# Optimization experiments

Measured on AMD Instinct MI355X. Metric: run time of the kernel, lower is better.

## Reference

```python
import jax, jax.numpy as jnp
import numpy as np

N_TOKENS = 16384
D_MODEL = 2048
N_BRANCH = 2
THRESHOLD = 0.5


def setup_inputs() -> dict:
    key = jax.random.key(0)
    k_x, k_w = jax.random.split(key)
    x = jax.random.normal(k_x, (N_TOKENS, D_MODEL), dtype=jnp.float32)
    gate_w = jax.random.normal(k_w, (D_MODEL, N_BRANCH), dtype=jnp.float32) / np.sqrt(D_MODEL)
    gate_b = jnp.zeros((N_BRANCH,), dtype=jnp.float32)
    return {"x": x, "gate_w": gate_w, "gate_b": gate_b}


def reference(x, gate_w, gate_b):
    # gate: linear + sigmoid -> per-branch scores in (0,1)
    score = jax.nn.sigmoid(x @ gate_w + gate_b)          # [N, 2]
    # threshold protocol: dispatch token to branch i iff score[:, i] > 0.5
    mask = (score > THRESHOLD).astype(x.dtype)           # [N, 2]
    s = score * mask                                     # routed scores (0 where not routed)

    # scatter to branches (experts are Identity), dense masked form
    x0 = x * mask[:, 0:1]                                # [N, D] tokens routed to branch 0
    x1 = x * mask[:, 1:2]                                # [N, D] tokens routed to branch 1
    s0 = s[:, 0:1]
    s1 = s[:, 1:2]

    # pre-combine weighting: weight each branch's tokens by its routed score, then combine (sum)
    pre_x = x0 * s0 + x1 * s1                            # [N, D]
    # post-combine weighting: combine tokens and scores separately, then multiply
    post_x = (x0 + x1) * (s0 + s1)                       # [N, D]
    return (pre_x, post_x)
```

## Files before the change

kernel.cpp:

```cpp
#include <hip/hip_runtime.h>

constexpr int N_TOKENS = 16384;
constexpr int D_MODEL  = 2048;

__global__ __launch_bounds__(256) void wbr_kernel(
    const float* __restrict__ x,
    const float* __restrict__ gw,
    const float* __restrict__ gb,
    float* __restrict__ out)
{
    const int row = blockIdx.x;
    const int t   = threadIdx.x;
    const size_t rbase = (size_t)row * D_MODEL;
    const float* xr = x + rbase;

    const int i0 = t * 4;
    const int i1 = 1024 + t * 4;

    const float4 xa = *reinterpret_cast<const float4*>(xr + i0);
    const float4 xb = *reinterpret_cast<const float4*>(xr + i1);

    const float4 wa0 = *reinterpret_cast<const float4*>(gw + 2 * i0);
    const float4 wa1 = *reinterpret_cast<const float4*>(gw + 2 * i0 + 4);
    const float4 wb0 = *reinterpret_cast<const float4*>(gw + 2 * i1);
    const float4 wb1 = *reinterpret_cast<const float4*>(gw + 2 * i1 + 4);

    double d0 = (double)xa.x * wa0.x + (double)xa.y * wa0.z
              + (double)xa.z * wa1.x + (double)xa.w * wa1.z
              + (double)xb.x * wb0.x + (double)xb.y * wb0.z
              + (double)xb.z * wb1.x + (double)xb.w * wb1.z;
    double d1 = (double)xa.x * wa0.y + (double)xa.y * wa0.w
              + (double)xa.z * wa1.y + (double)xa.w * wa1.w
              + (double)xb.x * wb0.y + (double)xb.y * wb0.w
              + (double)xb.z * wb1.y + (double)xb.w * wb1.w;

    #pragma unroll
    for (int off = 32; off > 0; off >>= 1) {
        d0 += __shfl_down(d0, off);
        d1 += __shfl_down(d1, off);
    }

    __shared__ double sred[4][2];
    __shared__ float  scl[2];
    const int wid = t >> 6;
    if ((t & 63) == 0) { sred[wid][0] = d0; sred[wid][1] = d1; }
    __syncthreads();
    if (t == 0) {
        const double z0 = sred[0][0] + sred[1][0] + sred[2][0] + sred[3][0] + (double)gb[0];
        const double z1 = sred[0][1] + sred[1][1] + sred[2][1] + sred[3][1] + (double)gb[1];
        const int m0 = z0 > 0.0;
        const int m1 = z1 > 0.0;
        const float s0 = m0 ? (float)(1.0 / (1.0 + exp(-z0))) : 0.0f;
        const float s1 = m1 ? (float)(1.0 / (1.0 + exp(-z1))) : 0.0f;
        const float a = s0 + s1;
        scl[0] = a;
        scl[1] = (float)(m0 + m1) * a;
    }
    __syncthreads();
    const float a = scl[0];
    const float b = scl[1];

    float* pre  = out + rbase;
    float* post = out + (size_t)N_TOKENS * D_MODEL + rbase;

    *reinterpret_cast<float4*>(pre + i0)  = make_float4(xa.x * a, xa.y * a, xa.z * a, xa.w * a);
    *reinterpret_cast<float4*>(pre + i1)  = make_float4(xb.x * a, xb.y * a, xb.z * a, xb.w * a);
    *reinterpret_cast<float4*>(post + i0) = make_float4(xa.x * b, xa.y * b, xa.z * b, xa.w * b);
    *reinterpret_cast<float4*>(post + i1) = make_float4(xb.x * b, xb.y * b, xb.z * b, xb.w * b);
}

extern "C" void kernel_launch(void* const* d_in, const int* in_sizes, int n_in,
                              void* d_out, int out_size, void* d_ws, size_t ws_size,
                              hipStream_t stream) {
    const float* x  = (const float*)d_in[0];
    const float* gw = (const float*)d_in[1];
    const float* gb = (const float*)d_in[2];
    float* out = (float*)d_out;
    wbr_kernel<<<N_TOKENS, 256, 0, stream>>>(x, gw, gb, out);
}
```

Before: 354.1 us.

## Map one wavefront per row and drop block-level shared-memory reduction

Each 64-lane wavefront now processes a whole token row, with 8 float4 loads per lane, and reduces with xor shuffles. This removes the shared-memory reduction and both block barriers. The sigmoid uses a single-precision fast exp instead of double exp. The cost is more registers per thread and slightly lower sigmoid precision.

New measurement: 360.6 us. No clear change (+1.8%).

```diff
diff --git a/kernel.cpp b/kernel.cpp
--- a/kernel.cpp
+++ b/kernel.cpp
@@ -9,64 +9,50 @@
     const float* __restrict__ gb,
     float* __restrict__ out)
 {
-    const int row = blockIdx.x;
-    const int t   = threadIdx.x;
+    const int lane = threadIdx.x & 63;
+    const int row  = (blockIdx.x << 2) | (threadIdx.x >> 6);
     const size_t rbase = (size_t)row * D_MODEL;
     const float* xr = x + rbase;
 
-    const int i0 = t * 4;
-    const int i1 = 1024 + t * 4;
-
-    const float4 xa = *reinterpret_cast<const float4*>(xr + i0);
-    const float4 xb = *reinterpret_cast<const float4*>(xr + i1);
-
-    const float4 wa0 = *reinterpret_cast<const float4*>(gw + 2 * i0);
-    const float4 wa1 = *reinterpret_cast<const float4*>(gw + 2 * i0 + 4);
-    const float4 wb0 = *reinterpret_cast<const float4*>(gw + 2 * i1);
-    const float4 wb1 = *reinterpret_cast<const float4*>(gw + 2 * i1 + 4);
-
-    double d0 = (double)xa.x * wa0.x + (double)xa.y * wa0.z
-              + (double)xa.z * wa1.x + (double)xa.w * wa1.z
-              + (double)xb.x * wb0.x + (double)xb.y * wb0.z
-              + (double)xb.z * wb1.x + (double)xb.w * wb1.z;
-    double d1 = (double)xa.x * wa0.y + (double)xa.y * wa0.w
-              + (double)xa.z * wa1.y + (double)xa.w * wa1.w
-              + (double)xb.x * wb0.y + (double)xb.y * wb0.w
-              + (double)xb.z * wb1.y + (double)xb.w * wb1.w;
+    float4 xv[8];
+    double d0 = 0.0, d1 = 0.0;
+    #pragma unroll
+    for (int k = 0; k < 8; ++k) {
+        const int e = (k << 8) + (lane << 2);
+        xv[k] = *reinterpret_cast<const float4*>(xr + e);
+        const float4 w0 = *reinterpret_cast<const float4*>(gw + 2 * e);
+        const float4 w1 = *reinterpret_cast<const float4*>(gw + 2 * e + 4);
+        d0 += (double)xv[k].x * w0.x + (double)xv[k].y * w0.z
+            + (double)xv[k].z * w1.x + (double)xv[k].w * w1.z;
+        d1 += (double)xv[k].x * w0.y + (double)xv[k].y * w0.w
+            + (double)xv[k].z * w1.y + (double)xv[k].w * w1.w;
+    }
 
     #pragma unroll
-    for (int off = 32; off > 0; off >>= 1) {
-        d0 += __shfl_down(d0, off);
-        d1 += __shfl_down(d1, off);
+    for (int off = 1; off < 64; off <<= 1) {
+        d0 += __shfl_xor(d0, off);
+        d1 += __shfl_xor(d1, off);
     }
 
-    __shared__ double sred[4][2];
-    __shared__ float  scl[2];
-    const int wid = t >> 6;
-    if ((t & 63) == 0) { sred[wid][0] = d0; sred[wid][1] = d1; }
-    __syncthreads();
-    if (t == 0) {
-        const double z0 = sred[0][0] + sred[1][0] + sred[2][0] + sred[3][0] + (double)gb[0];
-        const double z1 = sred[0][1] + sred[1][1] + sred[2][1] + sred[3][1] + (double)gb[1];
-        const int m0 = z0 > 0.0;
-        const int m1 = z1 > 0.0;
-        const float s0 = m0 ? (float)(1.0 / (1.0 + exp(-z0))) : 0.0f;
-        const float s1 = m1 ? (float)(1.0 / (1.0 + exp(-z1))) : 0.0f;
-        const float a = s0 + s1;
-        scl[0] = a;
-        scl[1] = (float)(m0 + m1) * a;
-    }
-    __syncthreads();
-    const float a = scl[0];
-    const float b = scl[1];
+    const double z0 = d0 + (double)gb[0];
+    const double z1 = d1 + (double)gb[1];
+    const int m0 = z0 > 0.0;
+    const int m1 = z1 > 0.0;
+    const float s0 = m0 ? 1.0f / (1.0f + __expf(-(float)z0)) : 0.0f;
+    const float s1 = m1 ? 1.0f / (1.0f + __expf(-(float)z1)) : 0.0f;
+    const float a = s0 + s1;
+    const float b = (float)(m0 + m1) * a;
 
     float* pre  = out + rbase;
     float* post = out + (size_t)N_TOKENS * D_MODEL + rbase;
-
-    *reinterpret_cast<float4*>(pre + i0)  = make_float4(xa.x * a, xa.y * a, xa.z * a, xa.w * a);
-    *reinterpret_cast<float4*>(pre + i1)  = make_float4(xb.x * a, xb.y * a, xb.z * a, xb.w * a);
-    *reinterpret_cast<float4*>(post + i0) = make_float4(xa.x * b, xa.y * b, xa.z * b, xa.w * b);
-    *reinterpret_cast<float4*>(post + i1) = make_float4(xb.x * b, xb.y * b, xb.z * b, xb.w * b);
+    #pragma unroll
+    for (int k = 0; k < 8; ++k) {
+        const int e = (k << 8) + (lane << 2);
+        *reinterpret_cast<float4*>(pre + e)  =
+            make_float4(xv[k].x * a, xv[k].y * a, xv[k].z * a, xv[k].w * a);
+        *reinterpret_cast<float4*>(post + e) =
+            make_float4(xv[k].x * b, xv[k].y * b, xv[k].z * b, xv[k].w * b);
+    }
 }
 
 extern "C" void kernel_launch(void* const* d_in, const int* in_sizes, int n_in,
@@ -76,5 +62,5 @@
     const float* gw = (const float*)d_in[1];
     const float* gb = (const float*)d_in[2];
     float* out = (float*)d_out;
-    wbr_kernel<<<N_TOKENS, 256, 0, stream>>>(x, gw, gb, out);
+    wbr_kernel<<<N_TOKENS / 4, 256, 0, stream>>>(x, gw, gb, out);
 }
```
